# Kernel tuning notes

Hardware: AMD Instinct MI355X
Metric: run time of the kernel (lower is better)

The kernel has to match this reference:

```python
import jax, jax.numpy as jnp
import numpy as np

H_FEATS = 256
N_NODES = 100000
N_EDGES = 1000000
EDGE_FEAT_DIM = 7
OUT_DIM = 4


def setup_inputs() -> dict:
    key = jax.random.key(0)
    ks = jax.random.split(key, 8)
    h = jax.random.normal(ks[0], (N_NODES, H_FEATS), dtype=jnp.float32)
    edge_feat = jax.random.normal(ks[1], (N_EDGES, EDGE_FEAT_DIM), dtype=jnp.float32)
    src = jax.random.randint(ks[2], (N_EDGES,), 0, N_NODES, dtype=jnp.int64)
    dst = jax.random.randint(ks[3], (N_EDGES,), 0, N_NODES, dtype=jnp.int64)
    in_dim = 2 * H_FEATS + EDGE_FEAT_DIM  # 519
    # Kaiming-ish init scale for the linear layers
    W1_w = jax.random.normal(ks[4], (in_dim, H_FEATS), dtype=jnp.float32) / np.sqrt(in_dim)
    W1_b = jax.random.normal(ks[5], (H_FEATS,), dtype=jnp.float32) * 0.01
    W2_w = jax.random.normal(ks[6], (H_FEATS, OUT_DIM), dtype=jnp.float32) / np.sqrt(H_FEATS)
    W2_b = jax.random.normal(ks[7], (OUT_DIM,), dtype=jnp.float32) * 0.01
    return {"h": h, "edge_feat": edge_feat, "src": src, "dst": dst,
            "W1_w": W1_w, "W1_b": W1_b, "W2_w": W2_w, "W2_b": W2_b}


def reference(h, edge_feat, src, dst, W1_w, W1_b, W2_w, W2_b):
    # Gather src/dst node embeddings per edge, concat with edge features: [E, 2*h_feats+7]
    x = jnp.concatenate([edge_feat, h[src], h[dst]], axis=1)
    # 2-layer MLP per edge: Linear -> ReLU -> Linear
    hid = jax.nn.relu(x @ W1_w + W1_b)          # [E, h_feats]
    rep = hid @ W2_w + W2_b                     # [E, 4]
    return rep
```

## Files before the change

### kernel.cpp

```cpp
#include <hip/hip_runtime.h>
#include <stdint.h>

#define NODES 100000
#define EDGES 1000000
#define HF 256
#define TILES (EDGES / 16)


typedef short short8 __attribute__((ext_vector_type(8)));
typedef float f32x4 __attribute__((ext_vector_type(4)));
typedef int i32x4 __attribute__((ext_vector_type(4)));

__device__ __forceinline__ unsigned short f2b(float f) {
  union { float f; uint32_t u; } v; v.f = f;
  return (unsigned short)((v.u + 0x7FFFu + ((v.u >> 16) & 1u)) >> 16);
}
__device__ __forceinline__ float b2f(unsigned short s) {
  union { uint32_t u; float f; } v; v.u = ((uint32_t)s) << 16;
  return v.f;
}

__global__ __launch_bounds__(256) void pack_w1(const float* __restrict__ W1,
                                               unsigned short* __restrict__ Bp) {
  int idx = blockIdx.x * 256 + threadIdx.x;
  int lane = idx & 63;
  int nbg  = (idx >> 6) & 31;
  int kb   = idx >> 11;
  int n    = nbg * 16 + (lane & 15);
  int k0   = kb * 32 + (lane >> 4) * 8;
  int rbase = (n < 256) ? 7 : 263;
  int col   = n & 255;
  short8 o;
#pragma unroll
  for (int j = 0; j < 8; ++j)
    o[j] = (short)f2b(W1[(size_t)(rbase + k0 + j) * HF + col]);
  *reinterpret_cast<short8*>(Bp + (size_t)idx * 8) = o;
}

__global__ __launch_bounds__(256) void gemm_R(const float* __restrict__ h,
                                              const unsigned short* __restrict__ Bp,
                                              const float* __restrict__ b1,
                                              unsigned short* __restrict__ R) {
  __shared__ unsigned short A[64][264];
  const int m0 = blockIdx.x * 64;
  const int t  = threadIdx.x;
  {
    const int r = t >> 2, q = t & 3;
    const int grow = m0 + r;
    const bool valid = grow < NODES;
    const float* hp = h + (size_t)grow * HF + q * 64;
#pragma unroll
    for (int cc = 0; cc < 8; ++cc) {
      float4 a, b;
      if (valid) {
        a = *reinterpret_cast<const float4*>(hp + cc * 8);
        b = *reinterpret_cast<const float4*>(hp + cc * 8 + 4);
      } else {
        a = make_float4(0.f, 0.f, 0.f, 0.f);
        b = a;
      }
      short8 o;
      o[0]=(short)f2b(a.x); o[1]=(short)f2b(a.y); o[2]=(short)f2b(a.z); o[3]=(short)f2b(a.w);
      o[4]=(short)f2b(b.x); o[5]=(short)f2b(b.y); o[6]=(short)f2b(b.z); o[7]=(short)f2b(b.w);
      *reinterpret_cast<short8*>(&A[r][q * 64 + cc * 8]) = o;
    }
  }
  __syncthreads();

  const int wave = t >> 6, lane = t & 63;
  const int l15 = lane & 15, lhi = lane >> 4;
  const int nbg0 = blockIdx.y * 16 + wave * 4;
  f32x4 acc[4][4] = {};
#pragma unroll
  for (int kb = 0; kb < 8; ++kb) {
    short8 bfrag[4];
#pragma unroll
    for (int nb = 0; nb < 4; ++nb)
      bfrag[nb] = *reinterpret_cast<const short8*>(
          Bp + (((size_t)(kb * 32 + nbg0 + nb) * 64 + lane) * 8));
    short8 afrag[4];
#pragma unroll
    for (int mb = 0; mb < 4; ++mb)
      afrag[mb] = *reinterpret_cast<const short8*>(&A[mb * 16 + l15][kb * 32 + lhi * 8]);
#pragma unroll
    for (int mb = 0; mb < 4; ++mb)
#pragma unroll
      for (int nb = 0; nb < 4; ++nb)
        acc[mb][nb] = __builtin_amdgcn_mfma_f32_16x16x32_bf16(
            afrag[mb], bfrag[nb], acc[mb][nb], 0, 0, 0);
  }
  const int c0 = blockIdx.y * 256 + wave * 64 + l15;
  float b1v[4] = {0.f, 0.f, 0.f, 0.f};
  if (blockIdx.y == 0) {
#pragma unroll
    for (int nb = 0; nb < 4; ++nb) b1v[nb] = b1[c0 + nb * 16];
  }
#pragma unroll
  for (int mb = 0; mb < 4; ++mb) {
#pragma unroll
    for (int i = 0; i < 4; ++i) {
      const int row = m0 + mb * 16 + lhi * 4 + i;
      if (row < NODES) {
        unsigned short* rp = R + (size_t)row * 512 + c0;
#pragma unroll
        for (int nb = 0; nb < 4; ++nb) rp[nb * 16] = f2b(acc[mb][nb][i] + b1v[nb]);
      }
    }
  }
}

__global__ __launch_bounds__(256) void edge_mlp(
    const unsigned short* __restrict__ R, const float* __restrict__ ef,
    const int* __restrict__ src, const int* __restrict__ dst,
    const float* __restrict__ W1, const float* __restrict__ W2,
    const float* __restrict__ b2, float* __restrict__ out) {
  __shared__ float w1a[7 * 256];
  for (int i = threadIdx.x; i < 7 * 64; i += 256)
    reinterpret_cast<float4*>(w1a)[i] = reinterpret_cast<const float4*>(W1)[i];
  __syncthreads();

  const int lane = threadIdx.x & 63;
  const int l15 = lane & 15, lhi = lane >> 4;

  short8 bfrag[8];
#pragma unroll
  for (int kb = 0; kb < 8; ++kb) {
    short8 b = {0, 0, 0, 0, 0, 0, 0, 0};
    if (l15 < 4) {
#pragma unroll
      for (int j = 0; j < 8; ++j)
        b[j] = (short)f2b(W2[(size_t)(kb * 32 + lhi * 8 + j) * 4 + l15]);
    }
    bfrag[kb] = b;
  }
  const float b2l = (l15 < 4) ? b2[l15] : 0.f;

  const int wid = (blockIdx.x * blockDim.x + threadIdx.x) >> 6;
  const int nw  = (gridDim.x * blockDim.x) >> 6;

  for (int t = wid; t < TILES; t += nw) {
    const int e0 = t * 16;
    const int ei = e0 + l15;
    const int s = src[ei];
    const int d = dst[ei];
    float efv[7];
#pragma unroll
    for (int j = 0; j < 7; ++j) efv[j] = ef[(size_t)ei * 7 + j];

    const unsigned short* Pp = R + (size_t)s * 512 + lhi * 8;
    const unsigned short* Qp = R + (size_t)d * 512 + 256 + lhi * 8;
    f32x4 acc = {};
#pragma unroll
    for (int kb = 0; kb < 8; ++kb) {
      const short8 pv = *reinterpret_cast<const short8*>(Pp + kb * 32);
      const short8 qv = *reinterpret_cast<const short8*>(Qp + kb * 32);
      float hd[8];
#pragma unroll
      for (int j2 = 0; j2 < 8; ++j2)
        hd[j2] = b2f((unsigned short)pv[j2]) + b2f((unsigned short)qv[j2]);
      const float* ws = w1a + kb * 32 + lhi * 8;
#pragma unroll
      for (int j = 0; j < 7; ++j) {
        const float4 wa = *reinterpret_cast<const float4*>(ws + j * 256);
        const float4 wb = *reinterpret_cast<const float4*>(ws + j * 256 + 4);
        hd[0] = fmaf(efv[j], wa.x, hd[0]);
        hd[1] = fmaf(efv[j], wa.y, hd[1]);
        hd[2] = fmaf(efv[j], wa.z, hd[2]);
        hd[3] = fmaf(efv[j], wa.w, hd[3]);
        hd[4] = fmaf(efv[j], wb.x, hd[4]);
        hd[5] = fmaf(efv[j], wb.y, hd[5]);
        hd[6] = fmaf(efv[j], wb.z, hd[6]);
        hd[7] = fmaf(efv[j], wb.w, hd[7]);
      }
      union { i32x4 i; short8 s8; } af;
#pragma unroll
      for (int w = 0; w < 4; ++w) {
        const float lo = fmaxf(hd[2 * w], 0.f);
        const float hi = fmaxf(hd[2 * w + 1], 0.f);
        uint32_t pk;
        asm("v_cvt_pk_bf16_f32 %0, %1, %2" : "=v"(pk) : "v"(lo), "v"(hi));
        af.i[w] = (int)pk;
      }
      acc = __builtin_amdgcn_mfma_f32_16x16x32_bf16(af.s8, bfrag[kb], acc, 0, 0, 0);
    }
    if (l15 < 4) {
#pragma unroll
      for (int i = 0; i < 4; ++i)
        out[(size_t)(e0 + lhi * 4 + i) * 4 + l15] = acc[i] + b2l;
    }
  }
}

extern "C" void kernel_launch(void* const* d_in, const int* in_sizes, int n_in,
                              void* d_out, int out_size, void* d_ws, size_t ws_size,
                              hipStream_t stream) {
  const float* h  = (const float*)d_in[0];
  const float* ef = (const float*)d_in[1];
  const int* src  = (const int*)d_in[2];
  const int* dst  = (const int*)d_in[3];
  const float* W1 = (const float*)d_in[4];
  const float* b1 = (const float*)d_in[5];
  const float* W2 = (const float*)d_in[6];
  const float* b2 = (const float*)d_in[7];
  float* out = (float*)d_out;

  const size_t bp_bytes = (size_t)8 * 32 * 64 * 8 * 2;
  unsigned short* Bp = (unsigned short*)d_ws;
  unsigned short* R  = (unsigned short*)((char*)d_ws + bp_bytes);

  pack_w1<<<64, 256, 0, stream>>>(W1, Bp);
  gemm_R<<<dim3((NODES + 63) / 64, 2), 256, 0, stream>>>(h, Bp, b1, R);
  edge_mlp<<<2048, 256, 0, stream>>>(R, ef, src, dst, W1, W2, b2, out);
}
```

Before: 248.1 us.

## Process two edge tiles per wave with prefetched gathers and packed FMA math

The edge MLP loop now handles 32 edges per wave iteration as two independent 16-edge tiles. It prefetches the gathered R rows two k-blocks ahead so more memory loads are in flight. The bf16 unpack and edge-feature FMAs use packed two-wide float vectors, and shared-memory W1 loads are reused across both tiles. The gemm_R staging swaps the software bf16 rounding for the hardware packed convert instruction. The cost is much higher register pressure, which may reduce occupancy.

Result: faster. 239.9 us (-3.3%).

```diff
diff --git a/kernel.cpp b/kernel.cpp
--- a/kernel.cpp
+++ b/kernel.cpp
@@ -4,20 +4,26 @@
 #define NODES 100000
 #define EDGES 1000000
 #define HF 256
-#define TILES (EDGES / 16)
+#define TILES2 (EDGES / 32)
 
 
 typedef short short8 __attribute__((ext_vector_type(8)));
 typedef float f32x4 __attribute__((ext_vector_type(4)));
+typedef float f32x2 __attribute__((ext_vector_type(2)));
 typedef int i32x4 __attribute__((ext_vector_type(4)));
 
 __device__ __forceinline__ unsigned short f2b(float f) {
   union { float f; uint32_t u; } v; v.f = f;
   return (unsigned short)((v.u + 0x7FFFu + ((v.u >> 16) & 1u)) >> 16);
 }
-__device__ __forceinline__ float b2f(unsigned short s) {
-  union { uint32_t u; float f; } v; v.u = ((uint32_t)s) << 16;
+__device__ __forceinline__ float asf(uint32_t u) {
+  union { uint32_t u; float f; } v; v.u = u;
   return v.f;
+}
+__device__ __forceinline__ uint32_t cvtpk(float lo, float hi) {
+  uint32_t pk;
+  asm("v_cvt_pk_bf16_f32 %0, %1, %2" : "=v"(pk) : "v"(lo), "v"(hi));
+  return pk;
 }
 
 __global__ __launch_bounds__(256) void pack_w1(const float* __restrict__ W1,
@@ -59,10 +65,13 @@
         a = make_float4(0.f, 0.f, 0.f, 0.f);
         b = a;
       }
-      short8 o;
-      o[0]=(short)f2b(a.x); o[1]=(short)f2b(a.y); o[2]=(short)f2b(a.z); o[3]=(short)f2b(a.w);
-      o[4]=(short)f2b(b.x); o[5]=(short)f2b(b.y); o[6]=(short)f2b(b.z); o[7]=(short)f2b(b.w);
-      *reinterpret_cast<short8*>(&A[r][q * 64 + cc * 8]) = o;
+      uint32_t o32[4];
+      o32[0] = cvtpk(a.x, a.y);
+      o32[1] = cvtpk(a.z, a.w);
+      o32[2] = cvtpk(b.x, b.y);
+      o32[3] = cvtpk(b.z, b.w);
+      *reinterpret_cast<uint4*>(&A[r][q * 64 + cc * 8]) =
+          make_uint4(o32[0], o32[1], o32[2], o32[3]);
     }
   }
   __syncthreads();
@@ -138,57 +147,90 @@
   const int wid = (blockIdx.x * blockDim.x + threadIdx.x) >> 6;
   const int nw  = (gridDim.x * blockDim.x) >> 6;
 
-  for (int t = wid; t < TILES; t += nw) {
-    const int e0 = t * 16;
-    const int ei = e0 + l15;
-    const int s = src[ei];
-    const int d = dst[ei];
-    float efv[7];
-#pragma unroll
-    for (int j = 0; j < 7; ++j) efv[j] = ef[(size_t)ei * 7 + j];
-
-    const unsigned short* Pp = R + (size_t)s * 512 + lhi * 8;
-    const unsigned short* Qp = R + (size_t)d * 512 + 256 + lhi * 8;
-    f32x4 acc = {};
+#define TILE_KB(PV, QV, EFV, ACC)                                              \
+  {                                                                            \
+    const uint32_t* pu = reinterpret_cast<const uint32_t*>(&PV);               \
+    const uint32_t* qu = reinterpret_cast<const uint32_t*>(&QV);               \
+    f32x2 hd[4];                                                               \
+    _Pragma("unroll") for (int w = 0; w < 4; ++w) {                            \
+      f32x2 p2 = {asf(pu[w] << 16), asf(pu[w] & 0xffff0000u)};                 \
+      f32x2 q2 = {asf(qu[w] << 16), asf(qu[w] & 0xffff0000u)};                 \
+      hd[w] = p2 + q2;                                                         \
+    }                                                                          \
+    _Pragma("unroll") for (int j = 0; j < 7; ++j) {                            \
+      f32x2 e2 = {EFV[j], EFV[j]};                                             \
+      hd[0] = wv[j][0] * e2 + hd[0];                                           \
+      hd[1] = wv[j][1] * e2 + hd[1];                                           \
+      hd[2] = wv[j][2] * e2 + hd[2];                                           \
+      hd[3] = wv[j][3] * e2 + hd[3];                                           \
+    }                                                                          \
+    union { i32x4 i; short8 s8; } af;                                          \
+    _Pragma("unroll") for (int w = 0; w < 4; ++w) {                            \
+      const float lo = fmaxf(hd[w][0], 0.f);                                   \
+      const float hi = fmaxf(hd[w][1], 0.f);                                   \
+      af.i[w] = (int)cvtpk(lo, hi);                                            \
+    }                                                                          \
+    ACC = __builtin_amdgcn_mfma_f32_16x16x32_bf16(af.s8, bfrag[kb], ACC, 0, 0, 0); \
+  }
+
+  for (int t = wid; t < TILES2; t += nw) {
+    const int e0 = t * 32;
+    const int eiA = e0 + l15;
+    const int eiB = eiA + 16;
+    const int sA = src[eiA], dA = dst[eiA];
+    const int sB = src[eiB], dB = dst[eiB];
+    float efA[7], efB[7];
+#pragma unroll
+    for (int j = 0; j < 7; ++j) {
+      efA[j] = ef[(size_t)eiA * 7 + j];
+      efB[j] = ef[(size_t)eiB * 7 + j];
+    }
+    const unsigned short* PpA = R + (size_t)sA * 512 + lhi * 8;
+    const unsigned short* QpA = R + (size_t)dA * 512 + 256 + lhi * 8;
+    const unsigned short* PpB = R + (size_t)sB * 512 + lhi * 8;
+    const unsigned short* QpB = R + (size_t)dB * 512 + 256 + lhi * 8;
+
+    short8 pA[8], qA[8], pB[8], qB[8];
+#pragma unroll
+    for (int kb = 0; kb < 2; ++kb) {
+      pA[kb] = *reinterpret_cast<const short8*>(PpA + kb * 32);
+      qA[kb] = *reinterpret_cast<const short8*>(QpA + kb * 32);
+      pB[kb] = *reinterpret_cast<const short8*>(PpB + kb * 32);
+      qB[kb] = *reinterpret_cast<const short8*>(QpB + kb * 32);
+    }
+
+    f32x4 accA = {}, accB = {};
 #pragma unroll
     for (int kb = 0; kb < 8; ++kb) {
-      const short8 pv = *reinterpret_cast<const short8*>(Pp + kb * 32);
-      const short8 qv = *reinterpret_cast<const short8*>(Qp + kb * 32);
-      float hd[8];
-#pragma unroll
-      for (int j2 = 0; j2 < 8; ++j2)
-        hd[j2] = b2f((unsigned short)pv[j2]) + b2f((unsigned short)qv[j2]);
+      if (kb < 6) {
+        pA[kb + 2] = *reinterpret_cast<const short8*>(PpA + (kb + 2) * 32);
+        qA[kb + 2] = *reinterpret_cast<const short8*>(QpA + (kb + 2) * 32);
+        pB[kb + 2] = *reinterpret_cast<const short8*>(PpB + (kb + 2) * 32);
+        qB[kb + 2] = *reinterpret_cast<const short8*>(QpB + (kb + 2) * 32);
+      }
+      f32x2 wv[7][4];
       const float* ws = w1a + kb * 32 + lhi * 8;
 #pragma unroll
       for (int j = 0; j < 7; ++j) {
         const float4 wa = *reinterpret_cast<const float4*>(ws + j * 256);
         const float4 wb = *reinterpret_cast<const float4*>(ws + j * 256 + 4);
-        hd[0] = fmaf(efv[j], wa.x, hd[0]);
-        hd[1] = fmaf(efv[j], wa.y, hd[1]);
-        hd[2] = fmaf(efv[j], wa.z, hd[2]);
-        hd[3] = fmaf(efv[j], wa.w, hd[3]);
-        hd[4] = fmaf(efv[j], wb.x, hd[4]);
-        hd[5] = fmaf(efv[j], wb.y, hd[5]);
-        hd[6] = fmaf(efv[j], wb.z, hd[6]);
-        hd[7] = fmaf(efv[j], wb.w, hd[7]);
-      }
-      union { i32x4 i; short8 s8; } af;
-#pragma unroll
-      for (int w = 0; w < 4; ++w) {
-        const float lo = fmaxf(hd[2 * w], 0.f);
-        const float hi = fmaxf(hd[2 * w + 1], 0.f);
-        uint32_t pk;
-        asm("v_cvt_pk_bf16_f32 %0, %1, %2" : "=v"(pk) : "v"(lo), "v"(hi));
-        af.i[w] = (int)pk;
-      }
-      acc = __builtin_amdgcn_mfma_f32_16x16x32_bf16(af.s8, bfrag[kb], acc, 0, 0, 0);
+        wv[j][0] = {wa.x, wa.y};
+        wv[j][1] = {wa.z, wa.w};
+        wv[j][2] = {wb.x, wb.y};
+        wv[j][3] = {wb.z, wb.w};
+      }
+      TILE_KB(pA[kb], qA[kb], efA, accA);
+      TILE_KB(pB[kb], qB[kb], efB, accB);
     }
     if (l15 < 4) {
 #pragma unroll
-      for (int i = 0; i < 4; ++i)
-        out[(size_t)(e0 + lhi * 4 + i) * 4 + l15] = acc[i] + b2l;
-    }
-  }
+      for (int i = 0; i < 4; ++i) {
+        out[(size_t)(e0 + lhi * 4 + i) * 4 + l15] = accA[i] + b2l;
+        out[(size_t)(e0 + 16 + lhi * 4 + i) * 4 + l15] = accB[i] + b2l;
+      }
+    }
+  }
+#undef TILE_KB
 }
 
 extern "C" void kernel_launch(void* const* d_in, const int* in_sizes, int n_in,
```
